# Optimization experiments

Hardware: AMD Instinct MI355X
Metric: run time of the kernel (lower is better)

The kernel has to match this reference:

```python
import jax, jax.numpy as jnp
import numpy as np

B = 262144
DIM = 128
TD = 32        # token_dim (per-token channel dim inside attention)
NT = DIM // TD # 4 tokens from x, +1 learnable -> N = 5
N = NT + 1
H = 8          # num_heads
HD = TD // H   # head_dim = 4
DEEP = 2


def setup_inputs() -> dict:
    key = jax.random.key(0)
    ks = jax.random.split(key, 7)
    x = jax.random.normal(ks[0], (B, DIM), dtype=jnp.float32)
    token = jax.random.normal(ks[1], (1, 1, TD), dtype=jnp.float32)
    # stacked per-layer params (DEEP layers)
    qkv_w = jax.random.normal(ks[2], (DEEP, 3 * TD, TD), dtype=jnp.float32) * (TD ** -0.5)
    qkv_b = jnp.zeros((DEEP, 3 * TD), dtype=jnp.float32)
    proj_w = jax.random.normal(ks[3], (DEEP, TD, TD), dtype=jnp.float32) * (TD ** -0.5)
    proj_b = jnp.zeros((DEEP, TD), dtype=jnp.float32)
    pos_bias = jax.random.normal(ks[4], (DEEP, H, N, N), dtype=jnp.float32)
    return {"x": x, "token": token, "qkv_w": qkv_w, "qkv_b": qkv_b,
            "proj_w": proj_w, "proj_b": proj_b, "pos_bias": pos_bias}


def reference(x, token, qkv_w, qkv_b, proj_w, proj_b, pos_bias):
    scale = HD ** -0.5
    b = x.shape[0]
    # split x into NT tokens of width TD, prepend learnable token -> [B, N, TD]
    y = jnp.concatenate(
        [jnp.broadcast_to(token, (b, 1, TD)), x.reshape(b, NT, TD)], axis=1)
    for i in range(DEEP):
        qkv = y @ qkv_w[i].T + qkv_b[i]                 # [B, N, 3*TD]
        qkv = qkv.reshape(b, N, 3, H, HD)
        q = qkv[:, :, 0].transpose(0, 2, 1, 3)          # [B, H, N, HD]
        k = qkv[:, :, 1].transpose(0, 2, 1, 3)
        v = qkv[:, :, 2].transpose(0, 2, 1, 3)
        attn = jnp.einsum('bhnd,bhmd->bhnm', q, k) * scale + pos_bias[i]
        attn = jax.nn.softmax(attn, axis=-1)
        o = jnp.einsum('bhnm,bhmd->bhnd', attn, v)      # [B, H, N, HD]
        o = o.transpose(0, 2, 1, 3).reshape(b, N, TD)
        y = y + (o @ proj_w[i].T + proj_b[i])           # residual
    return y[:, 0, :]                                   # [B, TD]
```

## Files before the change

kernel.cpp:

```cpp
#include <hip/hip_runtime.h>
#include <hip/hip_bf16.h>


#define NTOK 5

typedef decltype(__builtin_amdgcn_cvt_pkrtz(0.0f, 0.0f)) half2_t;
using half8_t = __attribute__((ext_vector_type(8))) _Float16;
using f32x4 = __attribute__((ext_vector_type(4))) float;

union H2 { half2_t h; unsigned int u; };
union H8 { half8_t h; uint4 u4; unsigned int u[4]; };

__device__ __forceinline__ half2_t u2h(unsigned int x) { H2 c; c.u = x; return c.h; }
__device__ __forceinline__ unsigned int h2u(half2_t h) { H2 c; c.h = h; return c.u; }
__device__ __forceinline__ unsigned int pk(float a, float b) {
  return h2u(__builtin_amdgcn_cvt_pkrtz(a, b));
}
__device__ __forceinline__ float bf2f(unsigned short u) {
  union { unsigned int u; float f; } c; c.u = ((unsigned int)u) << 16; return c.f;
}
__device__ __forceinline__ half2_t bfpair2h2(unsigned int u) {
  union { unsigned int u; float f; } lo, hi;
  lo.u = u << 16;
  hi.u = u & 0xffff0000u;
  return __builtin_amdgcn_cvt_pkrtz(lo.f, hi.f);
}
__device__ __forceinline__ unsigned int f2bfpair(float a, float b) {
  unsigned int ua = __float_as_uint(a), ub = __float_as_uint(b);
  ua = (ua + 0x7fffu + ((ua >> 16) & 1u)) >> 16;
  ub = (ub + 0x7fffu + ((ub >> 16) & 1u)) & 0xffff0000u;
  return ua | ub;
}

__device__ __forceinline__ int detect_bf16(const unsigned int* __restrict__ p) {
  int cnt = 0;
#pragma unroll
  for (int i = 0; i < 64; ++i) {
    unsigned int e = (p[i] >> 7) & 0xffu;
    cnt += (e >= 96u && e <= 150u) ? 1 : 0;
  }
  return (cnt >= 40) ? 1 : 0;
}

__global__ void prep_kernel(const void* __restrict__ xraw,
                            const void* __restrict__ qkv_w, const void* __restrict__ qkv_b,
                            const void* __restrict__ proj_w, const void* __restrict__ proj_b,
                            const void* __restrict__ pos_b,
                            unsigned int* __restrict__ wqkv, unsigned int* __restrict__ wproj,
                            float* __restrict__ bqkv, float* __restrict__ bproj,
                            float* __restrict__ pb, int* __restrict__ flag) {
  const int t = threadIdx.x;
  const int isbf = detect_bf16((const unsigned int*)xraw);
  if (t == 0) *flag = isbf;
  if (isbf) {
    const unsigned short* qw = (const unsigned short*)qkv_w;
    const unsigned short* qb = (const unsigned short*)qkv_b;
    const unsigned short* pw = (const unsigned short*)proj_w;
    const unsigned short* pbb = (const unsigned short*)proj_b;
    const unsigned short* pp = (const unsigned short*)pos_b;
    for (int i = t; i < 3072; i += 256)
      wqkv[i] = h2u(__builtin_amdgcn_cvt_pkrtz(bf2f(qw[2 * i]), bf2f(qw[2 * i + 1])));
    for (int i = t; i < 1024; i += 256)
      wproj[i] = h2u(__builtin_amdgcn_cvt_pkrtz(bf2f(pw[2 * i]), bf2f(pw[2 * i + 1])));
    for (int i = t; i < 192; i += 256) bqkv[i] = bf2f(qb[i]);
    for (int i = t; i < 64; i += 256) bproj[i] = bf2f(pbb[i]);
    for (int i = t; i < 400; i += 256) pb[i] = bf2f(pp[i]);
  } else {
    const float* qw = (const float*)qkv_w;
    const float* qb = (const float*)qkv_b;
    const float* pw = (const float*)proj_w;
    const float* pbb = (const float*)proj_b;
    const float* pp = (const float*)pos_b;
    for (int i = t; i < 3072; i += 256)
      wqkv[i] = h2u(__builtin_amdgcn_cvt_pkrtz(qw[2 * i], qw[2 * i + 1]));
    for (int i = t; i < 1024; i += 256)
      wproj[i] = h2u(__builtin_amdgcn_cvt_pkrtz(pw[2 * i], pw[2 * i + 1]));
    for (int i = t; i < 192; i += 256) bqkv[i] = qb[i];
    for (int i = t; i < 64; i += 256) bproj[i] = pbb[i];
    for (int i = t; i < 400; i += 256) pb[i] = pp[i];
  }
}

__device__ __forceinline__ half8_t ldfrag(const uint4* __restrict__ w, int row, int quad) {
  H8 c; c.u4 = w[row * 4 + quad]; return c.h;
}
__device__ __forceinline__ half8_t mk8(const unsigned int (&d)[4]) {
  H8 c; c.u[0] = d[0]; c.u[1] = d[1]; c.u[2] = d[2]; c.u[3] = d[3]; return c.h;
}

template <int TMIN>
__device__ __forceinline__ void qkv_token(const half8_t (&wa)[6], const f32x4 (&bias)[6],
                                          half8_t yb, unsigned int (&outdw)[6][2]) {
#pragma unroll
  for (int tile = TMIN; tile < 6; ++tile) {
    f32x4 acc = __builtin_amdgcn_mfma_f32_16x16x32_f16(wa[tile], yb, bias[tile], 0, 0, 0);
    outdw[tile][0] = pk(acc[0], acc[1]);
    outdw[tile][1] = pk(acc[2], acc[3]);
  }
}

template <int NR>
__device__ __forceinline__ void attention(const unsigned int (&dw)[NTOK][6][2],
                                          const float* __restrict__ pbl, int quad,
                                          unsigned int (&od)[2][NR][2]) {
#pragma unroll
  for (int s = 0; s < 2; ++s) {
    const float* pbh = pbl + (quad + 4 * s) * 25;
    float vf[NTOK][4];
#pragma unroll
    for (int m = 0; m < NTOK; ++m) {
      half2_t v0 = u2h(dw[m][4 + s][0]), v1 = u2h(dw[m][4 + s][1]);
      vf[m][0] = (float)v0.x; vf[m][1] = (float)v0.y;
      vf[m][2] = (float)v1.x; vf[m][3] = (float)v1.y;
    }
#pragma unroll
    for (int n = 0; n < NR; ++n) {
      float lg[NTOK];
#pragma unroll
      for (int m = 0; m < NTOK; ++m) {
        float d = __builtin_amdgcn_fdot2(u2h(dw[n][0 + s][0]), u2h(dw[m][2 + s][0]), 0.0f, false);
        d = __builtin_amdgcn_fdot2(u2h(dw[n][0 + s][1]), u2h(dw[m][2 + s][1]), d, false);
        lg[m] = fmaf(d, 0.5f, pbh[n * 5 + m]);
      }
      float mx = fmaxf(fmaxf(fmaxf(lg[0], lg[1]), fmaxf(lg[2], lg[3])), lg[4]);
      float e[NTOK], ssum = 0.0f;
#pragma unroll
      for (int m = 0; m < NTOK; ++m) {
        e[m] = __builtin_amdgcn_exp2f((lg[m] - mx) * 1.44269504f);
        ssum += e[m];
      }
      const float r = __builtin_amdgcn_rcpf(ssum);
      float o0 = 0.f, o1 = 0.f, o2 = 0.f, o3 = 0.f;
#pragma unroll
      for (int m = 0; m < NTOK; ++m) {
        o0 = fmaf(e[m], vf[m][0], o0); o1 = fmaf(e[m], vf[m][1], o1);
        o2 = fmaf(e[m], vf[m][2], o2); o3 = fmaf(e[m], vf[m][3], o3);
      }
      od[s][n][0] = pk(o0 * r, o1 * r);
      od[s][n][1] = pk(o2 * r, o3 * r);
    }
  }
}

__device__ __forceinline__ void regroup(int quad, int nl,
                                        unsigned int lo0, unsigned int lo1,
                                        unsigned int hi0, unsigned int hi1,
                                        unsigned int (&o)[4]) {
  const int sA = ((2 * quad) & 3) * 16 + nl;
  const int sB = ((2 * quad + 1) & 3) * 16 + nl;
  const unsigned int a0 = __shfl((int)lo0, sA, 64), a1 = __shfl((int)lo1, sA, 64);
  const unsigned int a2 = __shfl((int)hi0, sA, 64), a3 = __shfl((int)hi1, sA, 64);
  const unsigned int b0 = __shfl((int)lo0, sB, 64), b1 = __shfl((int)lo1, sB, 64);
  const unsigned int b2 = __shfl((int)hi0, sB, 64), b3 = __shfl((int)hi1, sB, 64);
  const bool hi = quad >= 2;
  o[0] = hi ? a2 : a0; o[1] = hi ? a3 : a1;
  o[2] = hi ? b2 : b0; o[3] = hi ? b3 : b1;
}

__global__ __launch_bounds__(256, 2) void vit_kernel(
    const void* __restrict__ x, const void* __restrict__ token,
    const unsigned int* __restrict__ wqkv, const unsigned int* __restrict__ wproj,
    const float* __restrict__ bqkv, const float* __restrict__ bproj,
    const float* __restrict__ pb, const int* __restrict__ flag,
    void* __restrict__ out) {
  const int tid = threadIdx.x;
  const int wave = tid >> 6, lane = tid & 63;
  const int quad = lane >> 4, nl = lane & 15;
  const size_t b = (size_t)blockIdx.x * 64 + wave * 16 + nl;
  const int isbf = *flag;

  unsigned int yd[NTOK][4];
  if (isbf) {
    const uint4 tk = *(const uint4*)((const unsigned short*)token + quad * 8);
    yd[0][0] = h2u(bfpair2h2(tk.x)); yd[0][1] = h2u(bfpair2h2(tk.y));
    yd[0][2] = h2u(bfpair2h2(tk.z)); yd[0][3] = h2u(bfpair2h2(tk.w));
#pragma unroll
    for (int t = 1; t < NTOK; ++t) {
      const uint4 u = *(const uint4*)((const unsigned short*)x + b * 128 + (t - 1) * 32 + quad * 8);
      yd[t][0] = h2u(bfpair2h2(u.x)); yd[t][1] = h2u(bfpair2h2(u.y));
      yd[t][2] = h2u(bfpair2h2(u.z)); yd[t][3] = h2u(bfpair2h2(u.w));
    }
  } else {
    const float4* tp = (const float4*)token;
    float4 a0 = tp[quad * 2], a1 = tp[quad * 2 + 1];
    yd[0][0] = pk(a0.x, a0.y); yd[0][1] = pk(a0.z, a0.w);
    yd[0][2] = pk(a1.x, a1.y); yd[0][3] = pk(a1.z, a1.w);
#pragma unroll
    for (int t = 1; t < NTOK; ++t) {
      const float4* xp = (const float4*)((const float*)x + b * 128 + (t - 1) * 32 + quad * 8);
      float4 u0 = xp[0], u1 = xp[1];
      yd[t][0] = pk(u0.x, u0.y); yd[t][1] = pk(u0.z, u0.w);
      yd[t][2] = pk(u1.x, u1.y); yd[t][3] = pk(u1.z, u1.w);
    }
  }

  const uint4* wq4 = (const uint4*)wqkv;
  const uint4* wp4 = (const uint4*)wproj;

  {
    half8_t wa[6]; f32x4 bias[6];
#pragma unroll
    for (int tile = 0; tile < 6; ++tile) {
      wa[tile] = ldfrag(wq4, tile * 16 + nl, quad);
      bias[tile] = *(const f32x4*)(bqkv + tile * 16 + quad * 4);
    }
    unsigned int dw[NTOK][6][2];
#pragma unroll
    for (int t = 0; t < NTOK; ++t) qkv_token<0>(wa, bias, mk8(yd[t]), dw[t]);

    unsigned int od[2][NTOK][2];
    attention<NTOK>(dw, pb, quad, od);

    half8_t wp[2]; f32x4 bp[2];
#pragma unroll
    for (int tile = 0; tile < 2; ++tile) {
      wp[tile] = ldfrag(wp4, tile * 16 + nl, quad);
      bp[tile] = *(const f32x4*)(bproj + tile * 16 + quad * 4);
    }
#pragma unroll
    for (int t = 0; t < NTOK; ++t) {
      unsigned int bfd[4];
      regroup(quad, nl, od[0][t][0], od[0][t][1], od[1][t][0], od[1][t][1], bfd);
      f32x4 p0 = __builtin_amdgcn_mfma_f32_16x16x32_f16(wp[0], mk8(bfd), bp[0], 0, 0, 0);
      f32x4 p1 = __builtin_amdgcn_mfma_f32_16x16x32_f16(wp[1], mk8(bfd), bp[1], 0, 0, 0);
      unsigned int pr[4];
      regroup(quad, nl, pk(p0[0], p0[1]), pk(p0[2], p0[3]), pk(p1[0], p1[1]), pk(p1[2], p1[3]), pr);
#pragma unroll
      for (int j = 0; j < 4; ++j) yd[t][j] = h2u(u2h(yd[t][j]) + u2h(pr[j]));
    }
  }

  {
    half8_t wa[6]; f32x4 bias[6];
#pragma unroll
    for (int tile = 0; tile < 6; ++tile) {
      wa[tile] = ldfrag(wq4, 96 + tile * 16 + nl, quad);
      bias[tile] = *(const f32x4*)(bqkv + 96 + tile * 16 + quad * 4);
    }
    unsigned int dw[NTOK][6][2];
    qkv_token<0>(wa, bias, mk8(yd[0]), dw[0]);
#pragma unroll
    for (int t = 1; t < NTOK; ++t) qkv_token<2>(wa, bias, mk8(yd[t]), dw[t]);

    unsigned int od[2][1][2];
    attention<1>(dw, pb + 200, quad, od);

    half8_t wp[2]; f32x4 bp[2];
#pragma unroll
    for (int tile = 0; tile < 2; ++tile) {
      wp[tile] = ldfrag(wp4, 32 + tile * 16 + nl, quad);
      bp[tile] = *(const f32x4*)(bproj + 32 + tile * 16 + quad * 4);
    }
    unsigned int bfd[4];
    regroup(quad, nl, od[0][0][0], od[0][0][1], od[1][0][0], od[1][0][1], bfd);
    f32x4 p0 = __builtin_amdgcn_mfma_f32_16x16x32_f16(wp[0], mk8(bfd), bp[0], 0, 0, 0);
    f32x4 p1 = __builtin_amdgcn_mfma_f32_16x16x32_f16(wp[1], mk8(bfd), bp[1], 0, 0, 0);

    unsigned int t0[4], t1[4];
    regroup(quad, nl, __float_as_uint(p0[0]), __float_as_uint(p0[1]),
            __float_as_uint(p1[0]), __float_as_uint(p1[1]), t0);
    regroup(quad, nl, __float_as_uint(p0[2]), __float_as_uint(p0[3]),
            __float_as_uint(p1[2]), __float_as_uint(p1[3]), t1);
    float pf[8] = {__uint_as_float(t0[0]), __uint_as_float(t0[1]),
                   __uint_as_float(t1[0]), __uint_as_float(t1[1]),
                   __uint_as_float(t0[2]), __uint_as_float(t0[3]),
                   __uint_as_float(t1[2]), __uint_as_float(t1[3])};
    float f[8];
#pragma unroll
    for (int j = 0; j < 4; ++j) {
      half2_t yv = u2h(yd[0][j]);
      f[2 * j + 0] = (float)yv.x + pf[2 * j + 0];
      f[2 * j + 1] = (float)yv.y + pf[2 * j + 1];
    }
    if (isbf) {
      uint4 r = make_uint4(f2bfpair(f[0], f[1]), f2bfpair(f[2], f[3]),
                           f2bfpair(f[4], f[5]), f2bfpair(f[6], f[7]));
      *(uint4*)((unsigned short*)out + b * 32 + quad * 8) = r;
    } else {
      float4* op = (float4*)((float*)out + b * 32 + quad * 8);
      op[0] = make_float4(f[0], f[1], f[2], f[3]);
      op[1] = make_float4(f[4], f[5], f[6], f[7]);
    }
  }
}

extern "C" void kernel_launch(void* const* d_in, const int* in_sizes, int n_in,
                              void* d_out, int out_size, void* d_ws, size_t ws_size,
                              hipStream_t stream) {
  const void* x      = d_in[0];
  const void* token  = d_in[1];
  const void* qkv_w  = d_in[2];
  const void* qkv_b  = d_in[3];
  const void* proj_w = d_in[4];
  const void* proj_b = d_in[5];
  const void* pos_b  = d_in[6];

  char* ws = (char*)d_ws;
  unsigned int* wqkv  = (unsigned int*)(ws + 0);
  unsigned int* wproj = (unsigned int*)(ws + 12288);
  float* bqkv  = (float*)(ws + 16384);
  float* bproj = (float*)(ws + 17152);
  float* pb    = (float*)(ws + 17408);
  int*   flag  = (int*)(ws + 19008);

  prep_kernel<<<1, 256, 0, stream>>>(x, qkv_w, qkv_b, proj_w, proj_b, pos_b,
                                     wqkv, wproj, bqkv, bproj, pb, flag);

  const int nrows = in_sizes[0] / 128;
  const int grid = nrows / 64;
  vit_kernel<<<grid, 256, 0, stream>>>(x, token, wqkv, wproj, bqkv, bproj, pb, flag, d_out);
}
```

Baseline: 240.0 us.

## Permute K dimension in weights and loads to remove cross-lane shuffles

Reorders the channel (K) dimension of the packed weights in the prep kernel and of the per-lane input loads. With matching orders, the attention output fragments and projection results already sit in the layout the next MFMA and the residual add expect. This removes the regroup shuffle sequences around every projection and the final output. It also raises launch bounds occupancy to 4 blocks per CU and runs the prep kernel on 8 blocks. Input and output accesses become two 8-byte or 16-byte pieces per lane instead of one contiguous chunk, which may reduce coalescing efficiency. The higher occupancy target may also force register spills.

```diff
diff --git a/kernel.cpp b/kernel.cpp
--- a/kernel.cpp
+++ b/kernel.cpp
@@ -49,36 +49,50 @@
                             unsigned int* __restrict__ wqkv, unsigned int* __restrict__ wproj,
                             float* __restrict__ bqkv, float* __restrict__ bproj,
                             float* __restrict__ pb, int* __restrict__ flag) {
-  const int t = threadIdx.x;
+  const int t = threadIdx.x + blockIdx.x * blockDim.x;
+  const int stride = blockDim.x * gridDim.x;
   const int isbf = detect_bf16((const unsigned int*)xraw);
   if (t == 0) *flag = isbf;
+#define PI_SRC(i, R, c0)                                    \
+  const int R = (i) >> 4;                                   \
+  const int q_ = ((i) >> 2) & 3, d_ = (i) & 3;              \
+  const int c0 = (d_ < 2) ? (4 * q_ + 2 * d_) : (16 + 4 * q_ + 2 * (d_ - 2));
   if (isbf) {
     const unsigned short* qw = (const unsigned short*)qkv_w;
     const unsigned short* qb = (const unsigned short*)qkv_b;
     const unsigned short* pw = (const unsigned short*)proj_w;
     const unsigned short* pbb = (const unsigned short*)proj_b;
     const unsigned short* pp = (const unsigned short*)pos_b;
-    for (int i = t; i < 3072; i += 256)
-      wqkv[i] = h2u(__builtin_amdgcn_cvt_pkrtz(bf2f(qw[2 * i]), bf2f(qw[2 * i + 1])));
-    for (int i = t; i < 1024; i += 256)
-      wproj[i] = h2u(__builtin_amdgcn_cvt_pkrtz(bf2f(pw[2 * i]), bf2f(pw[2 * i + 1])));
-    for (int i = t; i < 192; i += 256) bqkv[i] = bf2f(qb[i]);
-    for (int i = t; i < 64; i += 256) bproj[i] = bf2f(pbb[i]);
-    for (int i = t; i < 400; i += 256) pb[i] = bf2f(pp[i]);
+    for (int i = t; i < 3072; i += stride) {
+      PI_SRC(i, R, c0)
+      wqkv[i] = h2u(__builtin_amdgcn_cvt_pkrtz(bf2f(qw[R * 32 + c0]), bf2f(qw[R * 32 + c0 + 1])));
+    }
+    for (int i = t; i < 1024; i += stride) {
+      PI_SRC(i, R, c0)
+      wproj[i] = h2u(__builtin_amdgcn_cvt_pkrtz(bf2f(pw[R * 32 + c0]), bf2f(pw[R * 32 + c0 + 1])));
+    }
+    for (int i = t; i < 192; i += stride) bqkv[i] = bf2f(qb[i]);
+    for (int i = t; i < 64; i += stride) bproj[i] = bf2f(pbb[i]);
+    for (int i = t; i < 400; i += stride) pb[i] = bf2f(pp[i]);
   } else {
     const float* qw = (const float*)qkv_w;
     const float* qb = (const float*)qkv_b;
     const float* pw = (const float*)proj_w;
     const float* pbb = (const float*)proj_b;
     const float* pp = (const float*)pos_b;
-    for (int i = t; i < 3072; i += 256)
-      wqkv[i] = h2u(__builtin_amdgcn_cvt_pkrtz(qw[2 * i], qw[2 * i + 1]));
-    for (int i = t; i < 1024; i += 256)
-      wproj[i] = h2u(__builtin_amdgcn_cvt_pkrtz(pw[2 * i], pw[2 * i + 1]));
-    for (int i = t; i < 192; i += 256) bqkv[i] = qb[i];
-    for (int i = t; i < 64; i += 256) bproj[i] = pbb[i];
-    for (int i = t; i < 400; i += 256) pb[i] = pp[i];
-  }
+    for (int i = t; i < 3072; i += stride) {
+      PI_SRC(i, R, c0)
+      wqkv[i] = h2u(__builtin_amdgcn_cvt_pkrtz(qw[R * 32 + c0], qw[R * 32 + c0 + 1]));
+    }
+    for (int i = t; i < 1024; i += stride) {
+      PI_SRC(i, R, c0)
+      wproj[i] = h2u(__builtin_amdgcn_cvt_pkrtz(pw[R * 32 + c0], pw[R * 32 + c0 + 1]));
+    }
+    for (int i = t; i < 192; i += stride) bqkv[i] = qb[i];
+    for (int i = t; i < 64; i += stride) bproj[i] = pbb[i];
+    for (int i = t; i < 400; i += stride) pb[i] = pp[i];
+  }
+#undef PI_SRC
 }
 
 __device__ __forceinline__ half8_t ldfrag(const uint4* __restrict__ w, int row, int quad) {
@@ -102,7 +116,7 @@
 template <int NR>
 __device__ __forceinline__ void attention(const unsigned int (&dw)[NTOK][6][2],
                                           const float* __restrict__ pbl, int quad,
-                                          unsigned int (&od)[2][NR][2]) {
+                                          unsigned int (&od)[NR][4]) {
 #pragma unroll
   for (int s = 0; s < 2; ++s) {
     const float* pbh = pbl + (quad + 4 * s) * 25;
@@ -136,28 +150,13 @@
         o0 = fmaf(e[m], vf[m][0], o0); o1 = fmaf(e[m], vf[m][1], o1);
         o2 = fmaf(e[m], vf[m][2], o2); o3 = fmaf(e[m], vf[m][3], o3);
       }
-      od[s][n][0] = pk(o0 * r, o1 * r);
-      od[s][n][1] = pk(o2 * r, o3 * r);
-    }
-  }
-}
-
-__device__ __forceinline__ void regroup(int quad, int nl,
-                                        unsigned int lo0, unsigned int lo1,
-                                        unsigned int hi0, unsigned int hi1,
-                                        unsigned int (&o)[4]) {
-  const int sA = ((2 * quad) & 3) * 16 + nl;
-  const int sB = ((2 * quad + 1) & 3) * 16 + nl;
-  const unsigned int a0 = __shfl((int)lo0, sA, 64), a1 = __shfl((int)lo1, sA, 64);
-  const unsigned int a2 = __shfl((int)hi0, sA, 64), a3 = __shfl((int)hi1, sA, 64);
-  const unsigned int b0 = __shfl((int)lo0, sB, 64), b1 = __shfl((int)lo1, sB, 64);
-  const unsigned int b2 = __shfl((int)hi0, sB, 64), b3 = __shfl((int)hi1, sB, 64);
-  const bool hi = quad >= 2;
-  o[0] = hi ? a2 : a0; o[1] = hi ? a3 : a1;
-  o[2] = hi ? b2 : b0; o[3] = hi ? b3 : b1;
-}
-
-__global__ __launch_bounds__(256, 2) void vit_kernel(
+      od[n][2 * s + 0] = pk(o0 * r, o1 * r);
+      od[n][2 * s + 1] = pk(o2 * r, o3 * r);
+    }
+  }
+}
+
+__global__ __launch_bounds__(256, 4) void vit_kernel(
     const void* __restrict__ x, const void* __restrict__ token,
     const unsigned int* __restrict__ wqkv, const unsigned int* __restrict__ wproj,
     const float* __restrict__ bqkv, const float* __restrict__ bproj,
@@ -171,24 +170,26 @@
 
   unsigned int yd[NTOK][4];
   if (isbf) {
-    const uint4 tk = *(const uint4*)((const unsigned short*)token + quad * 8);
-    yd[0][0] = h2u(bfpair2h2(tk.x)); yd[0][1] = h2u(bfpair2h2(tk.y));
-    yd[0][2] = h2u(bfpair2h2(tk.z)); yd[0][3] = h2u(bfpair2h2(tk.w));
+    const unsigned short* tk = (const unsigned short*)token;
+    uint2 a0 = *(const uint2*)(tk + 4 * quad), a1 = *(const uint2*)(tk + 16 + 4 * quad);
+    yd[0][0] = h2u(bfpair2h2(a0.x)); yd[0][1] = h2u(bfpair2h2(a0.y));
+    yd[0][2] = h2u(bfpair2h2(a1.x)); yd[0][3] = h2u(bfpair2h2(a1.y));
 #pragma unroll
     for (int t = 1; t < NTOK; ++t) {
-      const uint4 u = *(const uint4*)((const unsigned short*)x + b * 128 + (t - 1) * 32 + quad * 8);
-      yd[t][0] = h2u(bfpair2h2(u.x)); yd[t][1] = h2u(bfpair2h2(u.y));
-      yd[t][2] = h2u(bfpair2h2(u.z)); yd[t][3] = h2u(bfpair2h2(u.w));
+      const unsigned short* xp = (const unsigned short*)x + b * 128 + (t - 1) * 32;
+      uint2 u0 = *(const uint2*)(xp + 4 * quad), u1 = *(const uint2*)(xp + 16 + 4 * quad);
+      yd[t][0] = h2u(bfpair2h2(u0.x)); yd[t][1] = h2u(bfpair2h2(u0.y));
+      yd[t][2] = h2u(bfpair2h2(u1.x)); yd[t][3] = h2u(bfpair2h2(u1.y));
     }
   } else {
-    const float4* tp = (const float4*)token;
-    float4 a0 = tp[quad * 2], a1 = tp[quad * 2 + 1];
+    const float* tk = (const float*)token;
+    float4 a0 = *(const float4*)(tk + 4 * quad), a1 = *(const float4*)(tk + 16 + 4 * quad);
     yd[0][0] = pk(a0.x, a0.y); yd[0][1] = pk(a0.z, a0.w);
     yd[0][2] = pk(a1.x, a1.y); yd[0][3] = pk(a1.z, a1.w);
 #pragma unroll
     for (int t = 1; t < NTOK; ++t) {
-      const float4* xp = (const float4*)((const float*)x + b * 128 + (t - 1) * 32 + quad * 8);
-      float4 u0 = xp[0], u1 = xp[1];
+      const float* xp = (const float*)x + b * 128 + (t - 1) * 32;
+      float4 u0 = *(const float4*)(xp + 4 * quad), u1 = *(const float4*)(xp + 16 + 4 * quad);
       yd[t][0] = pk(u0.x, u0.y); yd[t][1] = pk(u0.z, u0.w);
       yd[t][2] = pk(u1.x, u1.y); yd[t][3] = pk(u1.z, u1.w);
     }
@@ -208,7 +209,7 @@
 #pragma unroll
     for (int t = 0; t < NTOK; ++t) qkv_token<0>(wa, bias, mk8(yd[t]), dw[t]);
 
-    unsigned int od[2][NTOK][2];
+    unsigned int od[NTOK][4];
     attention<NTOK>(dw, pb, quad, od);
 
     half8_t wp[2]; f32x4 bp[2];
@@ -219,14 +220,12 @@
     }
 #pragma unroll
     for (int t = 0; t < NTOK; ++t) {
-      unsigned int bfd[4];
-      regroup(quad, nl, od[0][t][0], od[0][t][1], od[1][t][0], od[1][t][1], bfd);
-      f32x4 p0 = __builtin_amdgcn_mfma_f32_16x16x32_f16(wp[0], mk8(bfd), bp[0], 0, 0, 0);
-      f32x4 p1 = __builtin_amdgcn_mfma_f32_16x16x32_f16(wp[1], mk8(bfd), bp[1], 0, 0, 0);
-      unsigned int pr[4];
-      regroup(quad, nl, pk(p0[0], p0[1]), pk(p0[2], p0[3]), pk(p1[0], p1[1]), pk(p1[2], p1[3]), pr);
-#pragma unroll
-      for (int j = 0; j < 4; ++j) yd[t][j] = h2u(u2h(yd[t][j]) + u2h(pr[j]));
+      f32x4 p0 = __builtin_amdgcn_mfma_f32_16x16x32_f16(wp[0], mk8(od[t]), bp[0], 0, 0, 0);
+      f32x4 p1 = __builtin_amdgcn_mfma_f32_16x16x32_f16(wp[1], mk8(od[t]), bp[1], 0, 0, 0);
+      yd[t][0] = h2u(u2h(yd[t][0]) + u2h(pk(p0[0], p0[1])));
+      yd[t][1] = h2u(u2h(yd[t][1]) + u2h(pk(p0[2], p0[3])));
+      yd[t][2] = h2u(u2h(yd[t][2]) + u2h(pk(p1[0], p1[1])));
+      yd[t][3] = h2u(u2h(yd[t][3]) + u2h(pk(p1[2], p1[3])));
     }
   }
 
@@ -242,7 +241,7 @@
 #pragma unroll
     for (int t = 1; t < NTOK; ++t) qkv_token<2>(wa, bias, mk8(yd[t]), dw[t]);
 
-    unsigned int od[2][1][2];
+    unsigned int od[1][4];
     attention<1>(dw, pb + 200, quad, od);
 
     half8_t wp[2]; f32x4 bp[2];
@@ -251,35 +250,22 @@
       wp[tile] = ldfrag(wp4, 32 + tile * 16 + nl, quad);
       bp[tile] = *(const f32x4*)(bproj + 32 + tile * 16 + quad * 4);
     }
-    unsigned int bfd[4];
-    regroup(quad, nl, od[0][0][0], od[0][0][1], od[1][0][0], od[1][0][1], bfd);
-    f32x4 p0 = __builtin_amdgcn_mfma_f32_16x16x32_f16(wp[0], mk8(bfd), bp[0], 0, 0, 0);
-    f32x4 p1 = __builtin_amdgcn_mfma_f32_16x16x32_f16(wp[1], mk8(bfd), bp[1], 0, 0, 0);
-
-    unsigned int t0[4], t1[4];
-    regroup(quad, nl, __float_as_uint(p0[0]), __float_as_uint(p0[1]),
-            __float_as_uint(p1[0]), __float_as_uint(p1[1]), t0);
-    regroup(quad, nl, __float_as_uint(p0[2]), __float_as_uint(p0[3]),
-            __float_as_uint(p1[2]), __float_as_uint(p1[3]), t1);
-    float pf[8] = {__uint_as_float(t0[0]), __uint_as_float(t0[1]),
-                   __uint_as_float(t1[0]), __uint_as_float(t1[1]),
-                   __uint_as_float(t0[2]), __uint_as_float(t0[3]),
-                   __uint_as_float(t1[2]), __uint_as_float(t1[3])};
-    float f[8];
-#pragma unroll
-    for (int j = 0; j < 4; ++j) {
-      half2_t yv = u2h(yd[0][j]);
-      f[2 * j + 0] = (float)yv.x + pf[2 * j + 0];
-      f[2 * j + 1] = (float)yv.y + pf[2 * j + 1];
-    }
+    f32x4 p0 = __builtin_amdgcn_mfma_f32_16x16x32_f16(wp[0], mk8(od[0]), bp[0], 0, 0, 0);
+    f32x4 p1 = __builtin_amdgcn_mfma_f32_16x16x32_f16(wp[1], mk8(od[0]), bp[1], 0, 0, 0);
+
+    half2_t y0 = u2h(yd[0][0]), y1 = u2h(yd[0][1]), y2 = u2h(yd[0][2]), y3 = u2h(yd[0][3]);
+    float f[8] = {(float)y0.x + p0[0], (float)y0.y + p0[1],
+                  (float)y1.x + p0[2], (float)y1.y + p0[3],
+                  (float)y2.x + p1[0], (float)y2.y + p1[1],
+                  (float)y3.x + p1[2], (float)y3.y + p1[3]};
     if (isbf) {
-      uint4 r = make_uint4(f2bfpair(f[0], f[1]), f2bfpair(f[2], f[3]),
-                           f2bfpair(f[4], f[5]), f2bfpair(f[6], f[7]));
-      *(uint4*)((unsigned short*)out + b * 32 + quad * 8) = r;
+      unsigned short* op = (unsigned short*)out + b * 32;
+      *(uint2*)(op + 4 * quad) = make_uint2(f2bfpair(f[0], f[1]), f2bfpair(f[2], f[3]));
+      *(uint2*)(op + 16 + 4 * quad) = make_uint2(f2bfpair(f[4], f[5]), f2bfpair(f[6], f[7]));
     } else {
-      float4* op = (float4*)((float*)out + b * 32 + quad * 8);
-      op[0] = make_float4(f[0], f[1], f[2], f[3]);
-      op[1] = make_float4(f[4], f[5], f[6], f[7]);
+      float* op = (float*)out + b * 32;
+      *(float4*)(op + 4 * quad) = make_float4(f[0], f[1], f[2], f[3]);
+      *(float4*)(op + 16 + 4 * quad) = make_float4(f[4], f[5], f[6], f[7]);
     }
   }
 }
@@ -303,7 +289,7 @@
   float* pb    = (float*)(ws + 17408);
   int*   flag  = (int*)(ws + 19008);
 
-  prep_kernel<<<1, 256, 0, stream>>>(x, qkv_w, qkv_b, proj_w, proj_b, pos_b,
+  prep_kernel<<<8, 256, 0, stream>>>(x, qkv_w, qkv_b, proj_w, proj_b, pos_b,
                                      wqkv, wproj, bqkv, bproj, pb, flag);
 
   const int nrows = in_sizes[0] / 128;
```

Result: slower. 261.2 us (+8.8%).
